# Kernel optimization log

Measured on AMD Instinct MI355X. Metric: run time of the kernel, lower is better.

## Reference

```python
import jax, jax.numpy as jnp
import numpy as np

N, NFEAT, NHID = 10000, 128, 64


def _gc(x, adj, W, b):
    # GraphConvolution: adj @ (x @ W) + b
    return adj @ (x @ W) + b


def _fwd(x, adj, Wg0, bg0, Wg1, bg1, Wt0, bt0, Wt1, bt1,
         W000, b000, W001, b001, W100, b100, W101, b101,
         Wo0, bo0, Wo1, bo1, Wpp, bpp, Wpp2, bpp2, a, t):
    H = Wg0.shape[1]
    # outcome GCN stack (n_in=2), dropout is eval no-op
    rep_o = jax.nn.relu(_gc(x, adj, Wg0, bg0))
    rep_o = jax.nn.relu(_gc(rep_o, adj, Wg1, bg1))
    # treatment GCN stack
    rep_t = jax.nn.relu(_gc(x, adj, Wt0, bt0))
    rep_t = jax.nn.relu(_gc(rep_t, adj, Wt1, bt1))

    rep_cat = jnp.concatenate([rep_o, rep_t], axis=1)  # [N, 2H]
    # edge score(i,j) = [rep_cat_i ; rep_cat_j] @ a  =  s_src_i + s_dst_j
    s_src = rep_cat @ a[:2 * H, 0]   # [N]
    s_dst = rep_cat @ a[2 * H:, 0]   # [N]
    scores = s_src[:, None] + s_dst[None, :]          # [N, N]
    # only nonzero adj entries get a score; rest remain 0 (index_put into zeros)
    att = jnp.where(adj != 0, scores, jnp.zeros((), scores.dtype))
    att = jax.nn.softmax(att, axis=1)                 # full dense row softmax

    rep_out = att @ rep_t + rep_o                     # [N, H]

    treatment = jax.nn.sigmoid((rep_t @ Wpp + bpp) @ Wpp2 + bpp2)  # [N, 2]

    rep0 = rep_out
    rep1 = rep_out
    y00 = jax.nn.relu(rep0 @ W000 + b000)
    y10 = jax.nn.relu(rep1 @ W100 + b100)
    y00 = jax.nn.relu(y00 @ W001 + b001)
    y10 = jax.nn.relu(y10 @ W101 + b101)
    y0 = (y00 @ Wo0 + bo0).reshape(-1)
    y1 = (y10 @ Wo1 + bo1).reshape(-1)
    y = jnp.where(t > 0, y1, y0)
    return (y, rep_out, treatment)


def setup_inputs() -> dict:
    key = jax.random.key(0)
    ks = jax.random.split(key, 32)
    H = NHID
    x = jax.random.normal(ks[0], (N, NFEAT), dtype=jnp.float32)
    u = jax.random.uniform(ks[1], (N, N), dtype=jnp.float32)
    adj = jnp.where(u < 0.002, u, jnp.zeros((), jnp.float32))
    t = jax.random.randint(ks[2], (N,), 0, 2, dtype=jnp.int32)

    def lin(k, fi, fo):
        s = 1.0 / np.sqrt(fi)
        kw, kb = jax.random.split(k)
        return (jax.random.uniform(kw, (fi, fo), jnp.float32, -s, s),
                jax.random.uniform(kb, (fo,), jnp.float32, -s, s))

    Wg0, bg0 = lin(ks[3], NFEAT, H)
    Wg1, bg1 = lin(ks[4], H, H)
    Wt0, bt0 = lin(ks[5], NFEAT, H)
    Wt1, bt1 = lin(ks[6], H, H)
    W000, b000 = lin(ks[7], H, H)
    W001, b001 = lin(ks[8], H, H)
    W100, b100 = lin(ks[9], H, H)
    W101, b101 = lin(ks[10], H, H)
    Wo0, bo0 = lin(ks[11], H, 1)
    Wo1, bo1 = lin(ks[12], H, 1)
    Wpp, bpp = lin(ks[13], H, H)
    Wpp2, bpp2 = lin(ks[14], H, 2)
    # torch init is xavier with gain=0 (all zeros); use small random for a
    # meaningful correctness baseline
    a = jax.random.normal(ks[15], (4 * H, 1), dtype=jnp.float32) * 0.1
    return dict(x=x, adj=adj, t=t,
                Wg0=Wg0, bg0=bg0, Wg1=Wg1, bg1=bg1,
                Wt0=Wt0, bt0=bt0, Wt1=Wt1, bt1=bt1,
                W000=W000, b000=b000, W001=W001, b001=b001,
                W100=W100, b100=b100, W101=W101, b101=b101,
                Wo0=Wo0, bo0=bo0, Wo1=Wo1, bo1=bo1,
                Wpp=Wpp, bpp=bpp, Wpp2=Wpp2, bpp2=bpp2, a=a)


def reference(x, adj, t, Wg0, bg0, Wg1, bg1, Wt0, bt0, Wt1, bt1,
              W000, b000, W001, b001, W100, b100, W101, b101,
              Wo0, bo0, Wo1, bo1, Wpp, bpp, Wpp2, bpp2, a):
    return _fwd(x, adj, Wg0, bg0, Wg1, bg1, Wt0, bt0, Wt1, bt1,
                W000, b000, W001, b001, W100, b100, W101, b101,
                Wo0, bo0, Wo1, bo1, Wpp, bpp, Wpp2, bpp2, a, t)
```

## Files before the change

### kernel.cpp

```cpp
#include <hip/hip_runtime.h>
#include <hip/hip_bf16.h>

#define N_NODES 10000
#define ROW4    2500
#define CAP     64

#define OFF_CNT     0
#define OFF_COLSUM  10000
#define OFF_COLS    10064
#define OFF_VALS    650064
#define OFF_SSRC    1290064
#define OFF_SDST    1300064
#define OFF_B1      1310064
#define OFF_B2      1950064
#define OFF_B3      2590064
#define OFF_B4      3230064

__device__ __forceinline__ float wave_sum(float v) {
    #pragma unroll
    for (int off = 32; off >= 1; off >>= 1) v += __shfl_xor(v, off, 64);
    return v;
}
__device__ __forceinline__ float wave_max(float v) {
    #pragma unroll
    for (int off = 32; off >= 1; off >>= 1) v = fmaxf(v, __shfl_xor(v, off, 64));
    return v;
}

__global__ void k1_sparsify(const float4* __restrict__ adj4,
                            int* __restrict__ cnt,
                            int* __restrict__ cols,
                            float* __restrict__ vals,
                            float* __restrict__ colsum) {
    int tid = threadIdx.x;
    int row0 = blockIdx.x * 4;
    if (tid < 4) cnt[row0 + tid] = 0;
    if (blockIdx.x == 0 && tid < 64) colsum[tid] = 0.0f;
    __syncthreads();
    #pragma unroll
    for (int r = 0; r < 4; ++r) {
        int row = row0 + r;
        const float4* rp = adj4 + (size_t)row * ROW4;
        for (int idx = tid; idx < ROW4; idx += 256) {
            float4 v = rp[idx];
            float vv[4] = {v.x, v.y, v.z, v.w};
            #pragma unroll
            for (int l = 0; l < 4; ++l) {
                if (vv[l] != 0.0f) {
                    int pos = atomicAdd(&cnt[row], 1);
                    if (pos < CAP) {
                        cols[(size_t)row * CAP + pos] = idx * 4 + l;
                        vals[(size_t)row * CAP + pos] = vv[l];
                    }
                }
            }
        }
    }
}

__global__ void k2_gemm128(const float* __restrict__ x,
                           const float* __restrict__ Wg0,
                           const float* __restrict__ Wt0,
                           float* __restrict__ P, float* __restrict__ Q) {
    __shared__ float Ws[128 * 64];
    __shared__ float xs[8 * 128];
    int tid = threadIdx.x;
    int row0 = blockIdx.x * 8;
    ((float4*)xs)[tid] = ((const float4*)(x + (size_t)row0 * 128))[tid];
    for (int i = tid; i < 2048; i += 256) ((float4*)Ws)[i] = ((const float4*)Wg0)[i];
    __syncthreads();
    int sub = tid >> 6, f = tid & 63;
    float accP[2];
    #pragma unroll
    for (int g = 0; g < 2; ++g) {
        const float* xr = xs + (g * 4 + sub) * 128;
        float acc = 0.0f;
        #pragma unroll 8
        for (int k = 0; k < 128; k += 4) {
            float4 xv = *(const float4*)(xr + k);
            acc += xv.x * Ws[(k + 0) * 64 + f] + xv.y * Ws[(k + 1) * 64 + f]
                 + xv.z * Ws[(k + 2) * 64 + f] + xv.w * Ws[(k + 3) * 64 + f];
        }
        accP[g] = acc;
    }
    #pragma unroll
    for (int g = 0; g < 2; ++g)
        P[(size_t)(row0 + g * 4 + sub) * 64 + f] = accP[g];
    __syncthreads();
    for (int i = tid; i < 2048; i += 256) ((float4*)Ws)[i] = ((const float4*)Wt0)[i];
    __syncthreads();
    #pragma unroll
    for (int g = 0; g < 2; ++g) {
        const float* xr = xs + (g * 4 + sub) * 128;
        float acc = 0.0f;
        #pragma unroll 8
        for (int k = 0; k < 128; k += 4) {
            float4 xv = *(const float4*)(xr + k);
            acc += xv.x * Ws[(k + 0) * 64 + f] + xv.y * Ws[(k + 1) * 64 + f]
                 + xv.z * Ws[(k + 2) * 64 + f] + xv.w * Ws[(k + 3) * 64 + f];
        }
        Q[(size_t)(row0 + g * 4 + sub) * 64 + f] = acc;
    }
}

__global__ void k3_agg_gemm(const int* __restrict__ cnt, const int* __restrict__ cols,
                            const float* __restrict__ vals,
                            const float* __restrict__ P, const float* __restrict__ Q,
                            const float* __restrict__ bg0, const float* __restrict__ bt0,
                            const float* __restrict__ Wg1, const float* __restrict__ Wt1,
                            float* __restrict__ P2, float* __restrict__ Q2) {
    __shared__ float Wa[64 * 64], Wb[64 * 64];
    __shared__ float ra[8 * 64], rb[8 * 64];
    int tid = threadIdx.x, row0 = blockIdx.x * 8, sub = tid >> 6, f = tid & 63;
    for (int i = tid; i < 1024; i += 256) {
        ((float4*)Wa)[i] = ((const float4*)Wg1)[i];
        ((float4*)Wb)[i] = ((const float4*)Wt1)[i];
    }
    float bo = bg0[f], bt = bt0[f];
    #pragma unroll
    for (int g = 0; g < 2; ++g) {
        int lr = g * 4 + sub, row = row0 + lr;
        int c = min(cnt[row], CAP);
        const int* cp = cols + (size_t)row * CAP;
        const float* vp = vals + (size_t)row * CAP;
        float aP = 0.0f, aQ = 0.0f;
        for (int p = 0; p < c; ++p) {
            int col = cp[p]; float v = vp[p];
            aP += v * P[(size_t)col * 64 + f];
            aQ += v * Q[(size_t)col * 64 + f];
        }
        ra[lr * 64 + f] = fmaxf(aP + bo, 0.0f);
        rb[lr * 64 + f] = fmaxf(aQ + bt, 0.0f);
    }
    __syncthreads();
    #pragma unroll
    for (int g = 0; g < 2; ++g) {
        int lr = g * 4 + sub, row = row0 + lr;
        const float* rra = ra + lr * 64;
        const float* rrb = rb + lr * 64;
        float aA = 0.0f, aB = 0.0f;
        #pragma unroll 8
        for (int k = 0; k < 64; k += 4) {
            float4 va = *(const float4*)(rra + k);
            float4 vb = *(const float4*)(rrb + k);
            aA += va.x * Wa[(k + 0) * 64 + f] + va.y * Wa[(k + 1) * 64 + f]
                + va.z * Wa[(k + 2) * 64 + f] + va.w * Wa[(k + 3) * 64 + f];
            aB += vb.x * Wb[(k + 0) * 64 + f] + vb.y * Wb[(k + 1) * 64 + f]
                + vb.z * Wb[(k + 2) * 64 + f] + vb.w * Wb[(k + 3) * 64 + f];
        }
        P2[(size_t)row * 64 + f] = aA;
        Q2[(size_t)row * 64 + f] = aB;
    }
}

__global__ void k4_agg_score(const int* __restrict__ cnt, const int* __restrict__ cols,
                             const float* __restrict__ vals,
                             const float* __restrict__ P2, const float* __restrict__ Q2,
                             const float* __restrict__ bg1, const float* __restrict__ bt1,
                             const float* __restrict__ a,
                             const float* __restrict__ Wpp, const float* __restrict__ bpp,
                             const float* __restrict__ Wpp2, const float* __restrict__ bpp2,
                             float* __restrict__ rep_o, float* __restrict__ rep_t,
                             float* __restrict__ s_src, float* __restrict__ s_dst,
                             float* __restrict__ colsum, float* __restrict__ out_trt) {
    __shared__ float Wp[64 * 64];
    __shared__ float rts[8 * 64];
    int tid = threadIdx.x, row0 = blockIdx.x * 8, sub = tid >> 6, f = tid & 63;
    for (int i = tid; i < 1024; i += 256) ((float4*)Wp)[i] = ((const float4*)Wpp)[i];
    float bo = bg1[f], bt = bt1[f];
    float a0 = a[f], a1 = a[64 + f], a2 = a[128 + f], a3 = a[192 + f];
    #pragma unroll
    for (int g = 0; g < 2; ++g) {
        int lr = g * 4 + sub, row = row0 + lr;
        int c = min(cnt[row], CAP);
        const int* cp = cols + (size_t)row * CAP;
        const float* vp = vals + (size_t)row * CAP;
        float aO = 0.0f, aT = 0.0f;
        for (int p = 0; p < c; ++p) {
            int col = cp[p]; float v = vp[p];
            aO += v * P2[(size_t)col * 64 + f];
            aT += v * Q2[(size_t)col * 64 + f];
        }
        float vo = fmaxf(aO + bo, 0.0f);
        float vt = fmaxf(aT + bt, 0.0f);
        rep_o[(size_t)row * 64 + f] = vo;
        rep_t[(size_t)row * 64 + f] = vt;
        rts[lr * 64 + f] = vt;
        float ps = wave_sum(vo * a0 + vt * a1);
        float pd = wave_sum(vo * a2 + vt * a3);
        if (f == 0) { s_src[row] = ps; s_dst[row] = pd; }
    }
    __syncthreads();
    if (sub == 0) {
        float cs = 0.0f;
        #pragma unroll
        for (int lr = 0; lr < 8; ++lr) cs += rts[lr * 64 + f];
        atomicAdd(&colsum[f], cs);
    }
    float bp = bpp[f], w20 = Wpp2[f * 2 + 0], w21 = Wpp2[f * 2 + 1];
    #pragma unroll
    for (int g = 0; g < 2; ++g) {
        int lr = g * 4 + sub, row = row0 + lr;
        const float* rr = rts + lr * 64;
        float u = bp;
        #pragma unroll 8
        for (int k = 0; k < 64; k += 4) {
            float4 rv = *(const float4*)(rr + k);
            u += rv.x * Wp[(k + 0) * 64 + f] + rv.y * Wp[(k + 1) * 64 + f]
               + rv.z * Wp[(k + 2) * 64 + f] + rv.w * Wp[(k + 3) * 64 + f];
        }
        float p0 = wave_sum(u * w20);
        float p1 = wave_sum(u * w21);
        if (f == 0) {
            out_trt[(size_t)row * 2 + 0] = 1.0f / (1.0f + expf(-(p0 + bpp2[0])));
            out_trt[(size_t)row * 2 + 1] = 1.0f / (1.0f + expf(-(p1 + bpp2[1])));
        }
    }
}

__global__ void k5_attn_heads(const int* __restrict__ cnt, const int* __restrict__ cols,
                              const float* __restrict__ s_src, const float* __restrict__ s_dst,
                              const float* __restrict__ colsum,
                              const float* __restrict__ rep_o, const float* __restrict__ rep_t,
                              const float* __restrict__ W000, const float* __restrict__ b000,
                              const float* __restrict__ W001, const float* __restrict__ b001,
                              const float* __restrict__ W100, const float* __restrict__ b100,
                              const float* __restrict__ W101, const float* __restrict__ b101,
                              const float* __restrict__ Wo0, const float* __restrict__ bo0,
                              const float* __restrict__ Wo1, const float* __restrict__ bo1,
                              const int* __restrict__ t,
                              float* __restrict__ out_y, float* __restrict__ out_rep) {
    __shared__ float WA[64 * 64], WB[64 * 64];
    __shared__ float reps[8 * 64], u0s[8 * 64], u1s[8 * 64];
    int tid = threadIdx.x, row0 = blockIdx.x * 8, sub = tid >> 6, f = tid & 63;
    for (int i = tid; i < 1024; i += 256) {
        ((float4*)WA)[i] = ((const float4*)W000)[i];
        ((float4*)WB)[i] = ((const float4*)W100)[i];
    }
    float csf = colsum[f];
    #pragma unroll
    for (int g = 0; g < 2; ++g) {
        int lr = g * 4 + sub, row = row0 + lr;
        int c = min(cnt[row], CAP);
        const int* cp = cols + (size_t)row * CAP;
        float ssrc = s_src[row];
        int   col_l = (f < c) ? cp[f] : 0;
        float s_l   = (f < c) ? ssrc + s_dst[col_l] : -1e30f;
        float m = fmaxf(wave_max(s_l), 0.0f);
        float e_l = (f < c) ? expf(s_l - m) : 0.0f;
        float em = expf(-m);
        float Z = wave_sum(e_l) + (float)(N_NODES - c) * em;
        float acc = 0.0f;
        for (int p = 0; p < c; ++p) {
            float ep  = __shfl(e_l, p, 64);
            int  colp = __shfl(col_l, p, 64);
            acc += (ep - em) * rep_t[(size_t)colp * 64 + f];
        }
        float outv = (acc + em * csf) / Z + rep_o[(size_t)row * 64 + f];
        out_rep[(size_t)row * 64 + f] = outv;
        reps[lr * 64 + f] = outv;
    }
    __syncthreads();
    float bA = b000[f], bB = b100[f];
    #pragma unroll
    for (int g = 0; g < 2; ++g) {
        int lr = g * 4 + sub;
        const float* rr = reps + lr * 64;
        float u0 = bA, u1 = bB;
        #pragma unroll 8
        for (int k = 0; k < 64; k += 4) {
            float4 rv = *(const float4*)(rr + k);
            u0 += rv.x * WA[(k + 0) * 64 + f] + rv.y * WA[(k + 1) * 64 + f]
                + rv.z * WA[(k + 2) * 64 + f] + rv.w * WA[(k + 3) * 64 + f];
            u1 += rv.x * WB[(k + 0) * 64 + f] + rv.y * WB[(k + 1) * 64 + f]
                + rv.z * WB[(k + 2) * 64 + f] + rv.w * WB[(k + 3) * 64 + f];
        }
        u0s[lr * 64 + f] = fmaxf(u0, 0.0f);
        u1s[lr * 64 + f] = fmaxf(u1, 0.0f);
    }
    __syncthreads();
    for (int i = tid; i < 1024; i += 256) {
        ((float4*)WA)[i] = ((const float4*)W001)[i];
        ((float4*)WB)[i] = ((const float4*)W101)[i];
    }
    __syncthreads();
    float bC = b001[f], bD = b101[f], wo0 = Wo0[f], wo1 = Wo1[f];
    #pragma unroll
    for (int g = 0; g < 2; ++g) {
        int lr = g * 4 + sub, row = row0 + lr;
        const float* r0 = u0s + lr * 64;
        const float* r1 = u1s + lr * 64;
        float v0 = bC, v1 = bD;
        #pragma unroll 8
        for (int k = 0; k < 64; k += 4) {
            float4 a0 = *(const float4*)(r0 + k);
            float4 a1 = *(const float4*)(r1 + k);
            v0 += a0.x * WA[(k + 0) * 64 + f] + a0.y * WA[(k + 1) * 64 + f]
                + a0.z * WA[(k + 2) * 64 + f] + a0.w * WA[(k + 3) * 64 + f];
            v1 += a1.x * WB[(k + 0) * 64 + f] + a1.y * WB[(k + 1) * 64 + f]
                + a1.z * WB[(k + 2) * 64 + f] + a1.w * WB[(k + 3) * 64 + f];
        }
        float y0 = wave_sum(fmaxf(v0, 0.0f) * wo0);
        float y1 = wave_sum(fmaxf(v1, 0.0f) * wo1);
        if (f == 0)
            out_y[row] = (t[row] > 0) ? (y1 + bo1[0]) : (y0 + bo0[0]);
    }
}


extern "C" void kernel_launch(void* const* d_in, const int* in_sizes, int n_in,
                              void* d_out, int out_size, void* d_ws, size_t ws_size,
                              hipStream_t stream) {
    const float* x    = (const float*)d_in[0];
    const float* adj  = (const float*)d_in[1];
    const int*   t    = (const int*)d_in[2];
    const float* Wg0  = (const float*)d_in[3];
    const float* bg0  = (const float*)d_in[4];
    const float* Wg1  = (const float*)d_in[5];
    const float* bg1  = (const float*)d_in[6];
    const float* Wt0  = (const float*)d_in[7];
    const float* bt0  = (const float*)d_in[8];
    const float* Wt1  = (const float*)d_in[9];
    const float* bt1  = (const float*)d_in[10];
    const float* W000 = (const float*)d_in[11];
    const float* b000 = (const float*)d_in[12];
    const float* W001 = (const float*)d_in[13];
    const float* b001 = (const float*)d_in[14];
    const float* W100 = (const float*)d_in[15];
    const float* b100 = (const float*)d_in[16];
    const float* W101 = (const float*)d_in[17];
    const float* b101 = (const float*)d_in[18];
    const float* Wo0  = (const float*)d_in[19];
    const float* bo0  = (const float*)d_in[20];
    const float* Wo1  = (const float*)d_in[21];
    const float* bo1  = (const float*)d_in[22];
    const float* Wpp  = (const float*)d_in[23];
    const float* bpp  = (const float*)d_in[24];
    const float* Wpp2 = (const float*)d_in[25];
    const float* bpp2 = (const float*)d_in[26];
    const float* a    = (const float*)d_in[27];

    float* ws = (float*)d_ws;
    int*   cnt    = (int*)(ws + OFF_CNT);
    float* colsum = ws + OFF_COLSUM;
    int*   cols   = (int*)(ws + OFF_COLS);
    float* vals   = ws + OFF_VALS;
    float* s_src  = ws + OFF_SSRC;
    float* s_dst  = ws + OFF_SDST;
    float* B1     = ws + OFF_B1;
    float* B2     = ws + OFF_B2;
    float* B3     = ws + OFF_B3;
    float* B4     = ws + OFF_B4;

    float* out_y   = (float*)d_out;
    float* out_rep = (float*)d_out + N_NODES;
    float* out_trt = (float*)d_out + N_NODES + N_NODES * 64;

    k1_sparsify<<<2500, 256, 0, stream>>>((const float4*)adj, cnt, cols, vals, colsum);
    k2_gemm128<<<1250, 256, 0, stream>>>(x, Wg0, Wt0, B1, B2);
    k3_agg_gemm<<<1250, 256, 0, stream>>>(cnt, cols, vals, B1, B2, bg0, bt0, Wg1, Wt1, B3, B4);
    k4_agg_score<<<1250, 256, 0, stream>>>(cnt, cols, vals, B3, B4, bg1, bt1, a,
                                           Wpp, bpp, Wpp2, bpp2,
                                           B1, B2, s_src, s_dst, colsum, out_trt);
    k5_attn_heads<<<1250, 256, 0, stream>>>(cnt, cols, s_src, s_dst, colsum, B1, B2,
                                            W000, b000, W001, b001,
                                            W100, b100, W101, b101,
                                            Wo0, bo0, Wo1, bo1, t, out_y, out_rep);
}
```

Before: 774.8 us.

## Fuse sparsify with first GEMM, use wave-ballot compaction and shuffle-broadcast gathers

Merges the adjacency sparsification and the x@W GEMM into one launch, with separate block ranges for each job. Sparsification now gives each row to one wavefront and compacts nonzeros with ballot/popcount instead of global atomics. The aggregation loops load cols/vals into lanes once, broadcast them by shuffle, and keep several independent accumulators for more memory-level parallelism. Weight staging in shared memory is removed in favour of direct global/cached reads, which saves LDS and barriers but may cost more global load traffic.

```diff
diff --git a/kernel.cpp b/kernel.cpp
--- a/kernel.cpp
+++ b/kernel.cpp
@@ -4,6 +4,7 @@
 #define N_NODES 10000
 #define ROW4    2500
 #define CAP     64
+#define GEMM_BLOCKS 1250
 
 #define OFF_CNT     0
 #define OFF_COLSUM  10000
@@ -27,110 +28,97 @@
     return v;
 }
 
-__global__ void k1_sparsify(const float4* __restrict__ adj4,
-                            int* __restrict__ cnt,
-                            int* __restrict__ cols,
-                            float* __restrict__ vals,
-                            float* __restrict__ colsum) {
+__global__ void k1_fused(const float4* __restrict__ adj4, const float* __restrict__ x,
+                         const float* __restrict__ Wg0, const float* __restrict__ Wt0,
+                         int* __restrict__ cnt, int* __restrict__ cols,
+                         float* __restrict__ vals, float* __restrict__ colsum,
+                         float* __restrict__ P, float* __restrict__ Q) {
+    __shared__ float xs[8 * 128];
     int tid = threadIdx.x;
-    int row0 = blockIdx.x * 4;
-    if (tid < 4) cnt[row0 + tid] = 0;
-    if (blockIdx.x == 0 && tid < 64) colsum[tid] = 0.0f;
-    __syncthreads();
-    #pragma unroll
-    for (int r = 0; r < 4; ++r) {
-        int row = row0 + r;
+    if (blockIdx.x < GEMM_BLOCKS) {
+        int row0 = blockIdx.x * 8;
+        ((float4*)xs)[tid] = ((const float4*)(x + (size_t)row0 * 128))[tid];
+        if (blockIdx.x == 0 && tid < 64) colsum[tid] = 0.0f;
+        __syncthreads();
+        int sub = tid >> 6, f = tid & 63;
+        #pragma unroll
+        for (int g = 0; g < 2; ++g) {
+            const float* xr = xs + (g * 4 + sub) * 128;
+            float aP = 0.0f, aQ = 0.0f;
+            #pragma unroll 8
+            for (int k = 0; k < 128; k += 4) {
+                float4 xv = *(const float4*)(xr + k);
+                aP += xv.x * Wg0[(k + 0) * 64 + f] + xv.y * Wg0[(k + 1) * 64 + f]
+                    + xv.z * Wg0[(k + 2) * 64 + f] + xv.w * Wg0[(k + 3) * 64 + f];
+                aQ += xv.x * Wt0[(k + 0) * 64 + f] + xv.y * Wt0[(k + 1) * 64 + f]
+                    + xv.z * Wt0[(k + 2) * 64 + f] + xv.w * Wt0[(k + 3) * 64 + f];
+            }
+            P[(size_t)(row0 + g * 4 + sub) * 64 + f] = aP;
+            Q[(size_t)(row0 + g * 4 + sub) * 64 + f] = aQ;
+        }
+    } else {
+        int lane = tid & 63, w = tid >> 6;
+        int row = (blockIdx.x - GEMM_BLOCKS) * 4 + w;
         const float4* rp = adj4 + (size_t)row * ROW4;
-        for (int idx = tid; idx < ROW4; idx += 256) {
-            float4 v = rp[idx];
+        size_t base = (size_t)row * CAP;
+        int count = 0;
+        for (int it = 0; it < 40; ++it) {
+            int idx = it * 64 + lane;
+            float4 v = make_float4(0.f, 0.f, 0.f, 0.f);
+            if (idx < ROW4) v = rp[idx];
             float vv[4] = {v.x, v.y, v.z, v.w};
-            #pragma unroll
-            for (int l = 0; l < 4; ++l) {
-                if (vv[l] != 0.0f) {
-                    int pos = atomicAdd(&cnt[row], 1);
-                    if (pos < CAP) {
-                        cols[(size_t)row * CAP + pos] = idx * 4 + l;
-                        vals[(size_t)row * CAP + pos] = vv[l];
+            bool any = (v.x != 0.f) | (v.y != 0.f) | (v.z != 0.f) | (v.w != 0.f);
+            if (__ballot(any)) {
+                #pragma unroll
+                for (int l = 0; l < 4; ++l) {
+                    unsigned long long b = __ballot(vv[l] != 0.f);
+                    if (b) {
+                        int pre = __popcll(b & ((1ull << lane) - 1ull));
+                        if (vv[l] != 0.f) {
+                            int pos = count + pre;
+                            if (pos < CAP) {
+                                cols[base + pos] = idx * 4 + l;
+                                vals[base + pos] = vv[l];
+                            }
+                        }
+                        count += (int)__popcll(b);
                     }
                 }
             }
         }
-    }
-}
-
-__global__ void k2_gemm128(const float* __restrict__ x,
-                           const float* __restrict__ Wg0,
-                           const float* __restrict__ Wt0,
-                           float* __restrict__ P, float* __restrict__ Q) {
-    __shared__ float Ws[128 * 64];
-    __shared__ float xs[8 * 128];
-    int tid = threadIdx.x;
-    int row0 = blockIdx.x * 8;
-    ((float4*)xs)[tid] = ((const float4*)(x + (size_t)row0 * 128))[tid];
-    for (int i = tid; i < 2048; i += 256) ((float4*)Ws)[i] = ((const float4*)Wg0)[i];
-    __syncthreads();
-    int sub = tid >> 6, f = tid & 63;
-    float accP[2];
-    #pragma unroll
-    for (int g = 0; g < 2; ++g) {
-        const float* xr = xs + (g * 4 + sub) * 128;
-        float acc = 0.0f;
-        #pragma unroll 8
-        for (int k = 0; k < 128; k += 4) {
-            float4 xv = *(const float4*)(xr + k);
-            acc += xv.x * Ws[(k + 0) * 64 + f] + xv.y * Ws[(k + 1) * 64 + f]
-                 + xv.z * Ws[(k + 2) * 64 + f] + xv.w * Ws[(k + 3) * 64 + f];
-        }
-        accP[g] = acc;
-    }
-    #pragma unroll
-    for (int g = 0; g < 2; ++g)
-        P[(size_t)(row0 + g * 4 + sub) * 64 + f] = accP[g];
-    __syncthreads();
-    for (int i = tid; i < 2048; i += 256) ((float4*)Ws)[i] = ((const float4*)Wt0)[i];
-    __syncthreads();
-    #pragma unroll
-    for (int g = 0; g < 2; ++g) {
-        const float* xr = xs + (g * 4 + sub) * 128;
-        float acc = 0.0f;
-        #pragma unroll 8
-        for (int k = 0; k < 128; k += 4) {
-            float4 xv = *(const float4*)(xr + k);
-            acc += xv.x * Ws[(k + 0) * 64 + f] + xv.y * Ws[(k + 1) * 64 + f]
-                 + xv.z * Ws[(k + 2) * 64 + f] + xv.w * Ws[(k + 3) * 64 + f];
-        }
-        Q[(size_t)(row0 + g * 4 + sub) * 64 + f] = acc;
-    }
-}
-
-__global__ void k3_agg_gemm(const int* __restrict__ cnt, const int* __restrict__ cols,
+        if (lane == 0) cnt[row] = min(count, CAP);
+    }
+}
+
+__global__ void k2_agg_gemm(const int* __restrict__ cnt, const int* __restrict__ cols,
                             const float* __restrict__ vals,
                             const float* __restrict__ P, const float* __restrict__ Q,
                             const float* __restrict__ bg0, const float* __restrict__ bt0,
                             const float* __restrict__ Wg1, const float* __restrict__ Wt1,
                             float* __restrict__ P2, float* __restrict__ Q2) {
-    __shared__ float Wa[64 * 64], Wb[64 * 64];
     __shared__ float ra[8 * 64], rb[8 * 64];
     int tid = threadIdx.x, row0 = blockIdx.x * 8, sub = tid >> 6, f = tid & 63;
-    for (int i = tid; i < 1024; i += 256) {
-        ((float4*)Wa)[i] = ((const float4*)Wg1)[i];
-        ((float4*)Wb)[i] = ((const float4*)Wt1)[i];
-    }
     float bo = bg0[f], bt = bt0[f];
     #pragma unroll
     for (int g = 0; g < 2; ++g) {
         int lr = g * 4 + sub, row = row0 + lr;
         int c = min(cnt[row], CAP);
-        const int* cp = cols + (size_t)row * CAP;
-        const float* vp = vals + (size_t)row * CAP;
-        float aP = 0.0f, aQ = 0.0f;
-        for (int p = 0; p < c; ++p) {
-            int col = cp[p]; float v = vp[p];
-            aP += v * P[(size_t)col * 64 + f];
-            aQ += v * Q[(size_t)col * 64 + f];
-        }
-        ra[lr * 64 + f] = fmaxf(aP + bo, 0.0f);
-        rb[lr * 64 + f] = fmaxf(aQ + bt, 0.0f);
+        float v_l = 0.0f; int c_l = 0;
+        if (f < c) { c_l = cols[(size_t)row * CAP + f]; v_l = vals[(size_t)row * CAP + f]; }
+        float a0 = 0.f, a1 = 0.f, b0 = 0.f, b1 = 0.f;
+        for (int p = 0; p < c; p += 8) {
+            #pragma unroll
+            for (int j = 0; j < 8; j += 2) {
+                float vv0 = __shfl(v_l, p + j, 64);     int cc0 = __shfl(c_l, p + j, 64);
+                float vv1 = __shfl(v_l, p + j + 1, 64); int cc1 = __shfl(c_l, p + j + 1, 64);
+                a0 += vv0 * P[(size_t)cc0 * 64 + f];
+                b0 += vv0 * Q[(size_t)cc0 * 64 + f];
+                a1 += vv1 * P[(size_t)cc1 * 64 + f];
+                b1 += vv1 * Q[(size_t)cc1 * 64 + f];
+            }
+        }
+        ra[lr * 64 + f] = fmaxf(a0 + a1 + bo, 0.0f);
+        rb[lr * 64 + f] = fmaxf(b0 + b1 + bt, 0.0f);
     }
     __syncthreads();
     #pragma unroll
@@ -138,22 +126,22 @@
         int lr = g * 4 + sub, row = row0 + lr;
         const float* rra = ra + lr * 64;
         const float* rrb = rb + lr * 64;
-        float aA = 0.0f, aB = 0.0f;
+        float aA = 0.f, aB = 0.f;
         #pragma unroll 8
         for (int k = 0; k < 64; k += 4) {
             float4 va = *(const float4*)(rra + k);
             float4 vb = *(const float4*)(rrb + k);
-            aA += va.x * Wa[(k + 0) * 64 + f] + va.y * Wa[(k + 1) * 64 + f]
-                + va.z * Wa[(k + 2) * 64 + f] + va.w * Wa[(k + 3) * 64 + f];
-            aB += vb.x * Wb[(k + 0) * 64 + f] + vb.y * Wb[(k + 1) * 64 + f]
-                + vb.z * Wb[(k + 2) * 64 + f] + vb.w * Wb[(k + 3) * 64 + f];
+            aA += va.x * Wg1[(k + 0) * 64 + f] + va.y * Wg1[(k + 1) * 64 + f]
+                + va.z * Wg1[(k + 2) * 64 + f] + va.w * Wg1[(k + 3) * 64 + f];
+            aB += vb.x * Wt1[(k + 0) * 64 + f] + vb.y * Wt1[(k + 1) * 64 + f]
+                + vb.z * Wt1[(k + 2) * 64 + f] + vb.w * Wt1[(k + 3) * 64 + f];
         }
         P2[(size_t)row * 64 + f] = aA;
         Q2[(size_t)row * 64 + f] = aB;
     }
 }
 
-__global__ void k4_agg_score(const int* __restrict__ cnt, const int* __restrict__ cols,
+__global__ void k3_agg_score(const int* __restrict__ cnt, const int* __restrict__ cols,
                              const float* __restrict__ vals,
                              const float* __restrict__ P2, const float* __restrict__ Q2,
                              const float* __restrict__ bg1, const float* __restrict__ bt1,
@@ -163,31 +151,35 @@
                              float* __restrict__ rep_o, float* __restrict__ rep_t,
                              float* __restrict__ s_src, float* __restrict__ s_dst,
                              float* __restrict__ colsum, float* __restrict__ out_trt) {
-    __shared__ float Wp[64 * 64];
     __shared__ float rts[8 * 64];
     int tid = threadIdx.x, row0 = blockIdx.x * 8, sub = tid >> 6, f = tid & 63;
-    for (int i = tid; i < 1024; i += 256) ((float4*)Wp)[i] = ((const float4*)Wpp)[i];
     float bo = bg1[f], bt = bt1[f];
-    float a0 = a[f], a1 = a[64 + f], a2 = a[128 + f], a3 = a[192 + f];
+    float a0c = a[f], a1c = a[64 + f], a2c = a[128 + f], a3c = a[192 + f];
     #pragma unroll
     for (int g = 0; g < 2; ++g) {
         int lr = g * 4 + sub, row = row0 + lr;
         int c = min(cnt[row], CAP);
-        const int* cp = cols + (size_t)row * CAP;
-        const float* vp = vals + (size_t)row * CAP;
-        float aO = 0.0f, aT = 0.0f;
-        for (int p = 0; p < c; ++p) {
-            int col = cp[p]; float v = vp[p];
-            aO += v * P2[(size_t)col * 64 + f];
-            aT += v * Q2[(size_t)col * 64 + f];
-        }
-        float vo = fmaxf(aO + bo, 0.0f);
-        float vt = fmaxf(aT + bt, 0.0f);
+        float v_l = 0.0f; int c_l = 0;
+        if (f < c) { c_l = cols[(size_t)row * CAP + f]; v_l = vals[(size_t)row * CAP + f]; }
+        float a0 = 0.f, a1 = 0.f, b0 = 0.f, b1 = 0.f;
+        for (int p = 0; p < c; p += 8) {
+            #pragma unroll
+            for (int j = 0; j < 8; j += 2) {
+                float vv0 = __shfl(v_l, p + j, 64);     int cc0 = __shfl(c_l, p + j, 64);
+                float vv1 = __shfl(v_l, p + j + 1, 64); int cc1 = __shfl(c_l, p + j + 1, 64);
+                a0 += vv0 * P2[(size_t)cc0 * 64 + f];
+                b0 += vv0 * Q2[(size_t)cc0 * 64 + f];
+                a1 += vv1 * P2[(size_t)cc1 * 64 + f];
+                b1 += vv1 * Q2[(size_t)cc1 * 64 + f];
+            }
+        }
+        float vo = fmaxf(a0 + a1 + bo, 0.0f);
+        float vt = fmaxf(b0 + b1 + bt, 0.0f);
         rep_o[(size_t)row * 64 + f] = vo;
         rep_t[(size_t)row * 64 + f] = vt;
         rts[lr * 64 + f] = vt;
-        float ps = wave_sum(vo * a0 + vt * a1);
-        float pd = wave_sum(vo * a2 + vt * a3);
+        float ps = wave_sum(vo * a0c + vt * a1c);
+        float pd = wave_sum(vo * a2c + vt * a3c);
         if (f == 0) { s_src[row] = ps; s_dst[row] = pd; }
     }
     __syncthreads();
@@ -206,8 +198,8 @@
         #pragma unroll 8
         for (int k = 0; k < 64; k += 4) {
             float4 rv = *(const float4*)(rr + k);
-            u += rv.x * Wp[(k + 0) * 64 + f] + rv.y * Wp[(k + 1) * 64 + f]
-               + rv.z * Wp[(k + 2) * 64 + f] + rv.w * Wp[(k + 3) * 64 + f];
+            u += rv.x * Wpp[(k + 0) * 64 + f] + rv.y * Wpp[(k + 1) * 64 + f]
+               + rv.z * Wpp[(k + 2) * 64 + f] + rv.w * Wpp[(k + 3) * 64 + f];
         }
         float p0 = wave_sum(u * w20);
         float p1 = wave_sum(u * w21);
@@ -218,7 +210,7 @@
     }
 }
 
-__global__ void k5_attn_heads(const int* __restrict__ cnt, const int* __restrict__ cols,
+__global__ void k4_attn_heads(const int* __restrict__ cnt, const int* __restrict__ cols,
                               const float* __restrict__ s_src, const float* __restrict__ s_dst,
                               const float* __restrict__ colsum,
                               const float* __restrict__ rep_o, const float* __restrict__ rep_t,
@@ -230,33 +222,36 @@
                               const float* __restrict__ Wo1, const float* __restrict__ bo1,
                               const int* __restrict__ t,
                               float* __restrict__ out_y, float* __restrict__ out_rep) {
-    __shared__ float WA[64 * 64], WB[64 * 64];
     __shared__ float reps[8 * 64], u0s[8 * 64], u1s[8 * 64];
     int tid = threadIdx.x, row0 = blockIdx.x * 8, sub = tid >> 6, f = tid & 63;
-    for (int i = tid; i < 1024; i += 256) {
-        ((float4*)WA)[i] = ((const float4*)W000)[i];
-        ((float4*)WB)[i] = ((const float4*)W100)[i];
-    }
     float csf = colsum[f];
     #pragma unroll
     for (int g = 0; g < 2; ++g) {
         int lr = g * 4 + sub, row = row0 + lr;
         int c = min(cnt[row], CAP);
-        const int* cp = cols + (size_t)row * CAP;
         float ssrc = s_src[row];
-        int   col_l = (f < c) ? cp[f] : 0;
+        int   col_l = (f < c) ? cols[(size_t)row * CAP + f] : 0;
         float s_l   = (f < c) ? ssrc + s_dst[col_l] : -1e30f;
         float m = fmaxf(wave_max(s_l), 0.0f);
         float e_l = (f < c) ? expf(s_l - m) : 0.0f;
         float em = expf(-m);
         float Z = wave_sum(e_l) + (float)(N_NODES - c) * em;
-        float acc = 0.0f;
-        for (int p = 0; p < c; ++p) {
-            float ep  = __shfl(e_l, p, 64);
-            int  colp = __shfl(col_l, p, 64);
-            acc += (ep - em) * rep_t[(size_t)colp * 64 + f];
-        }
-        float outv = (acc + em * csf) / Z + rep_o[(size_t)row * 64 + f];
+        float g_l = (f < c) ? (e_l - em) : 0.0f;
+        float a0 = 0.f, a1 = 0.f, a2 = 0.f, a3 = 0.f;
+        for (int p = 0; p < c; p += 8) {
+            #pragma unroll
+            for (int j = 0; j < 8; j += 4) {
+                float g0 = __shfl(g_l, p + j + 0, 64); int c0 = __shfl(col_l, p + j + 0, 64);
+                float g1 = __shfl(g_l, p + j + 1, 64); int c1 = __shfl(col_l, p + j + 1, 64);
+                float g2 = __shfl(g_l, p + j + 2, 64); int c2 = __shfl(col_l, p + j + 2, 64);
+                float g3 = __shfl(g_l, p + j + 3, 64); int c3 = __shfl(col_l, p + j + 3, 64);
+                a0 += g0 * rep_t[(size_t)c0 * 64 + f];
+                a1 += g1 * rep_t[(size_t)c1 * 64 + f];
+                a2 += g2 * rep_t[(size_t)c2 * 64 + f];
+                a3 += g3 * rep_t[(size_t)c3 * 64 + f];
+            }
+        }
+        float outv = ((a0 + a1 + a2 + a3) + em * csf) / Z + rep_o[(size_t)row * 64 + f];
         out_rep[(size_t)row * 64 + f] = outv;
         reps[lr * 64 + f] = outv;
     }
@@ -270,18 +265,13 @@
         #pragma unroll 8
         for (int k = 0; k < 64; k += 4) {
             float4 rv = *(const float4*)(rr + k);
-            u0 += rv.x * WA[(k + 0) * 64 + f] + rv.y * WA[(k + 1) * 64 + f]
-                + rv.z * WA[(k + 2) * 64 + f] + rv.w * WA[(k + 3) * 64 + f];
-            u1 += rv.x * WB[(k + 0) * 64 + f] + rv.y * WB[(k + 1) * 64 + f]
-                + rv.z * WB[(k + 2) * 64 + f] + rv.w * WB[(k + 3) * 64 + f];
+            u0 += rv.x * W000[(k + 0) * 64 + f] + rv.y * W000[(k + 1) * 64 + f]
+                + rv.z * W000[(k + 2) * 64 + f] + rv.w * W000[(k + 3) * 64 + f];
+            u1 += rv.x * W100[(k + 0) * 64 + f] + rv.y * W100[(k + 1) * 64 + f]
+                + rv.z * W100[(k + 2) * 64 + f] + rv.w * W100[(k + 3) * 64 + f];
         }
         u0s[lr * 64 + f] = fmaxf(u0, 0.0f);
         u1s[lr * 64 + f] = fmaxf(u1, 0.0f);
-    }
-    __syncthreads();
-    for (int i = tid; i < 1024; i += 256) {
-        ((float4*)WA)[i] = ((const float4*)W001)[i];
-        ((float4*)WB)[i] = ((const float4*)W101)[i];
     }
     __syncthreads();
     float bC = b001[f], bD = b101[f], wo0 = Wo0[f], wo1 = Wo1[f];
@@ -293,12 +283,12 @@
         float v0 = bC, v1 = bD;
         #pragma unroll 8
         for (int k = 0; k < 64; k += 4) {
-            float4 a0 = *(const float4*)(r0 + k);
-            float4 a1 = *(const float4*)(r1 + k);
-            v0 += a0.x * WA[(k + 0) * 64 + f] + a0.y * WA[(k + 1) * 64 + f]
-                + a0.z * WA[(k + 2) * 64 + f] + a0.w * WA[(k + 3) * 64 + f];
-            v1 += a1.x * WB[(k + 0) * 64 + f] + a1.y * WB[(k + 1) * 64 + f]
-                + a1.z * WB[(k + 2) * 64 + f] + a1.w * WB[(k + 3) * 64 + f];
+            float4 q0 = *(const float4*)(r0 + k);
+            float4 q1 = *(const float4*)(r1 + k);
+            v0 += q0.x * W001[(k + 0) * 64 + f] + q0.y * W001[(k + 1) * 64 + f]
+                + q0.z * W001[(k + 2) * 64 + f] + q0.w * W001[(k + 3) * 64 + f];
+            v1 += q1.x * W101[(k + 0) * 64 + f] + q1.y * W101[(k + 1) * 64 + f]
+                + q1.z * W101[(k + 2) * 64 + f] + q1.w * W101[(k + 3) * 64 + f];
         }
         float y0 = wave_sum(fmaxf(v0, 0.0f) * wo0);
         float y1 = wave_sum(fmaxf(v1, 0.0f) * wo1);
@@ -356,13 +346,13 @@
     float* out_rep = (float*)d_out + N_NODES;
     float* out_trt = (float*)d_out + N_NODES + N_NODES * 64;
 
-    k1_sparsify<<<2500, 256, 0, stream>>>((const float4*)adj, cnt, cols, vals, colsum);
-    k2_gemm128<<<1250, 256, 0, stream>>>(x, Wg0, Wt0, B1, B2);
-    k3_agg_gemm<<<1250, 256, 0, stream>>>(cnt, cols, vals, B1, B2, bg0, bt0, Wg1, Wt1, B3, B4);
-    k4_agg_score<<<1250, 256, 0, stream>>>(cnt, cols, vals, B3, B4, bg1, bt1, a,
+    k1_fused<<<GEMM_BLOCKS + 2500, 256, 0, stream>>>((const float4*)adj, x, Wg0, Wt0,
+                                                     cnt, cols, vals, colsum, B1, B2);
+    k2_agg_gemm<<<1250, 256, 0, stream>>>(cnt, cols, vals, B1, B2, bg0, bt0, Wg1, Wt1, B3, B4);
+    k3_agg_score<<<1250, 256, 0, stream>>>(cnt, cols, vals, B3, B4, bg1, bt1, a,
                                            Wpp, bpp, Wpp2, bpp2,
                                            B1, B2, s_src, s_dst, colsum, out_trt);
-    k5_attn_heads<<<1250, 256, 0, stream>>>(cnt, cols, s_src, s_dst, colsum, B1, B2,
+    k4_attn_heads<<<1250, 256, 0, stream>>>(cnt, cols, s_src, s_dst, colsum, B1, B2,
                                             W000, b000, W001, b001,
                                             W100, b100, W101, b101,
                                             Wo0, bo0, Wo1, bo1, t, out_y, out_rep);
```

Measured after the change: 690.4 us. 1.12x faster.
